# Performance work log

Measured on AMD Instinct MI355X. Metric: run time of the kernel, lower is better.

The kernel has to match this reference:

```python
import jax, jax.numpy as jnp
import numpy as np

N_NODES = 100000
N_EDGES = 1600000
HID = 128
N_GRAPHS = 2048


def _glorot(key, shape):
    fan_in, fan_out = shape[0], shape[1]
    lim = (6.0 / (fan_in + fan_out)) ** 0.5
    return jax.random.uniform(key, shape, jnp.float32, -lim, lim)


def setup_inputs() -> dict:
    key = jax.random.key(0)
    ks = jax.random.split(key, 16)
    x = jax.random.normal(ks[0], (N_NODES, 1), jnp.float32)
    edge_index = jax.random.randint(ks[1], (2, N_EDGES), 0, N_NODES, jnp.int64)
    batch = jnp.sort(jax.random.randint(ks[2], (N_NODES,), 0, N_GRAPHS, jnp.int64))
    return {
        "x": x,
        "edge_index": edge_index,
        "batch": batch,
        "W1": _glorot(ks[3], (1, HID)),   "b1": jnp.zeros((HID,), jnp.float32),
        "W2": _glorot(ks[4], (HID, HID)), "b2": jnp.zeros((HID,), jnp.float32),
        "W3": _glorot(ks[5], (HID, HID)), "b3": jnp.zeros((HID,), jnp.float32),
        "Wl1": _glorot(ks[6], (HID, HID)), "bl1": jnp.zeros((HID,), jnp.float32),
        "Wl2": _glorot(ks[7], (HID, HID)), "bl2": jnp.zeros((HID,), jnp.float32),
        "Wl3": _glorot(ks[8], (HID, 1)),   "bl3": jnp.zeros((1,), jnp.float32),
    }


def _gcn_layer(h, src, dst, norm, W, b, n_nodes):
    # h: [N, Fin] -> [N, Fout]; GCNConv: D^-1/2 (A+I) D^-1/2 (h W) + b
    hw = h @ W                                   # [N, Fout]
    msg = hw[src] * norm[:, None]                # [E+N, Fout] gather + scale
    return jax.ops.segment_sum(msg, dst, num_segments=n_nodes) + b


def _gcn_norm(edge_index, n_nodes, dtype):
    loop = jnp.arange(n_nodes, dtype=edge_index.dtype)
    src = jnp.concatenate([edge_index[0], loop])  # self-loops appended
    dst = jnp.concatenate([edge_index[1], loop])
    deg = jax.ops.segment_sum(jnp.ones_like(dst, dtype=dtype), dst, num_segments=n_nodes)
    dinv = jnp.where(deg > 0, jax.lax.rsqrt(jnp.maximum(deg, 1e-12)), 0.0)
    norm = dinv[src] * dinv[dst]                  # [E+N]
    return src, dst, norm


def reference(x, edge_index, batch, W1, b1, W2, b2, W3, b3, Wl1, bl1, Wl2, bl2, Wl3, bl3):
    n = x.shape[0]
    src, dst, norm = _gcn_norm(edge_index, n, x.dtype)
    h = jax.nn.relu(_gcn_layer(x, src, dst, norm, W1, b1, n))
    h = jax.nn.relu(_gcn_layer(h, src, dst, norm, W2, b2, n))
    h = jax.nn.relu(_gcn_layer(h, src, dst, norm, W3, b3, n))
    # global_mean_pool over graph ids
    sums = jax.ops.segment_sum(h, batch, num_segments=N_GRAPHS)          # [G, HID]
    cnt = jax.ops.segment_sum(jnp.ones((n,), h.dtype), batch, num_segments=N_GRAPHS)
    g = sums / jnp.maximum(cnt, 1.0)[:, None]
    g = jax.nn.relu(g @ Wl1 + bl1)
    g = jax.nn.relu(g @ Wl2 + bl2)
    out = g @ Wl3 + bl3                                                  # [G, 1]
    return out.reshape(-1)
```

## Files before the change

### kernel.cpp

```cpp
#include <hip/hip_runtime.h>
#include <hip/hip_fp16.h>

#define H 128
#define SHIFT 9
#define BN 512
#define MAXNB 256
#define CHUNK 4096
#define CAP 16384

typedef _Float16 half8 __attribute__((ext_vector_type(8)));
typedef _Float16 half4 __attribute__((ext_vector_type(4)));
typedef _Float16 half2t __attribute__((ext_vector_type(2)));
typedef float f32x4 __attribute__((ext_vector_type(4)));


__global__ __launch_bounds__(256) void scatter_pairs_k(const int* __restrict__ src,
                                                       const int* __restrict__ dst,
                                                       int* __restrict__ gcur,
                                                       unsigned* __restrict__ pairbuf,
                                                       int E, int NBv) {
    __shared__ unsigned stage[CHUNK];
    __shared__ unsigned char stb[CHUNK];
    __shared__ int hist[MAXNB], basel[MAXNB], cur[MAXNB], gbase[MAXNB];
    __shared__ int total;
    int tid = threadIdx.x;
    int base = blockIdx.x * CHUNK;

    int mysrc[16], mydst[16];
    #pragma unroll
    for (int i = 0; i < 16; ++i) {
        int e = base + i * 256 + tid;
        if (e < E) { mysrc[i] = src[e]; mydst[i] = dst[e]; } else mydst[i] = -1;
    }
    hist[tid] = 0;
    __syncthreads();
    #pragma unroll
    for (int i = 0; i < 16; ++i)
        if (mydst[i] >= 0) atomicAdd(&hist[mydst[i] >> SHIFT], 1);
    __syncthreads();
    if (tid == 0) {
        int run = 0;
        for (int b = 0; b < NBv; ++b) { basel[b] = run; run += hist[b]; }
        total = run;
    }
    __syncthreads();
    if (tid < NBv) {
        cur[tid] = basel[tid];
        if (hist[tid] > 0) gbase[tid] = tid * CAP + atomicAdd(&gcur[tid], hist[tid]);
    }
    __syncthreads();
    #pragma unroll
    for (int i = 0; i < 16; ++i)
        if (mydst[i] >= 0) {
            int b = mydst[i] >> SHIFT;
            int slot = atomicAdd(&cur[b], 1);
            stage[slot] = ((unsigned)(mydst[i] & (BN - 1)) << 17) | (unsigned)mysrc[i];
            stb[slot] = (unsigned char)b;
        }
    __syncthreads();
    for (int s = tid; s < total; s += 256) {
        int b = stb[s];
        pairbuf[gbase[b] + (s - basel[b])] = stage[s];
    }
}

__global__ __launch_bounds__(512) void build_csr_k(const unsigned* __restrict__ pairbuf,
                                                   const int* __restrict__ gcur,
                                                   const float* __restrict__ x,
                                                   int* __restrict__ offs, int* __restrict__ eend,
                                                   float* __restrict__ dinv, float* __restrict__ s,
                                                   int* __restrict__ csr, int N) {
    __shared__ int hist[BN];
    __shared__ int cur[BN];
    __shared__ int ps[BN];
    int b = blockIdx.x, tid = threadIdx.x;
    int node0 = b << SHIFT;
    int e0 = b * CAP, e1 = e0 + gcur[b];
    hist[tid] = 0;
    __syncthreads();
    for (int p = e0 + tid; p < e1; p += 512)
        atomicAdd(&hist[pairbuf[p] >> 17], 1);
    __syncthreads();
    int v0 = hist[tid];
    ps[tid] = v0;
    __syncthreads();
    for (int off = 1; off < BN; off <<= 1) {
        int t = (tid >= off) ? ps[tid - off] : 0;
        __syncthreads();
        ps[tid] += t;
        __syncthreads();
    }
    int g0 = e0 + ps[tid] - v0;
    int n0 = node0 + tid;
    if (n0 < N) {
        float d = rsqrtf((float)(v0 + 1));
        offs[n0] = g0;
        eend[n0] = g0 + v0;
        dinv[n0] = d;
        s[n0] = x[n0] * d;
    }
    cur[tid] = g0;
    __syncthreads();
    for (int p = e0 + tid; p < e1; p += 512) {
        unsigned v = pairbuf[p];
        int pos = atomicAdd(&cur[v >> 17], 1);
        csr[pos] = (int)(v & 0x1FFFFu);
    }
}


__global__ __launch_bounds__(256) void agg1_k(const float* __restrict__ s, const int* __restrict__ offs,
                                              const int* __restrict__ eend, const int* __restrict__ csr,
                                              const float* __restrict__ dinv, float2* __restrict__ td, int n) {
    int l = threadIdx.x & 63;
    int wave = threadIdx.x >> 6;
    int sub = l >> 4;
    int j   = l & 15;
    int node = blockIdx.x * 16 + wave * 4 + sub;
    int nd = node < n ? node : n - 1;
    int e0 = offs[nd], e1 = eend[nd];
    float sum = 0.f;
    int p = e0 + j;
    for (; p + 16 < e1; p += 32) {
        int iA = csr[p];
        int iB = csr[p + 16];
        float vA = s[iA];
        float vB = s[iB];
        sum += vA + vB;
    }
    if (p < e1) sum += s[csr[p]];
    #pragma unroll
    for (int m = 1; m < 16; m <<= 1) sum += __shfl_xor(sum, m);
    if (j == 0 && node < n) {
        float d = dinv[nd];
        td[node] = make_float2((sum + s[nd]) * d, d);
    }
}


__global__ __launch_bounds__(256) void gather_td_k(const int* __restrict__ csr,
                                                   const float2* __restrict__ td,
                                                   const int* __restrict__ gcur,
                                                   float2* __restrict__ etd) {
    int b = blockIdx.x >> 2;
    int k = blockIdx.x & 3;
    int base = b * CAP + k * (CAP / 4);
    int e1 = b * CAP + gcur[b];
    int hi = base + (CAP / 4); if (hi > e1) hi = e1;
    for (int p0 = base; p0 < hi; p0 += 1024) {
        int p = p0 + threadIdx.x;
        bool m0 = (p < hi), m1 = (p + 256 < hi), m2 = (p + 512 < hi), m3 = (p + 768 < hi);
        int i0 = m0 ? csr[p] : 0;
        int i1 = m1 ? csr[p + 256] : 0;
        int i2 = m2 ? csr[p + 512] : 0;
        int i3 = m3 ? csr[p + 768] : 0;
        float2 v0 = td[i0];
        float2 v1 = td[i1];
        float2 v2 = td[i2];
        float2 v3 = td[i3];
        if (m0) etd[p] = v0;
        if (m1) etd[p + 256] = v1;
        if (m2) etd[p + 512] = v2;
        if (m3) etd[p + 768] = v3;
    }
}


__global__ __launch_bounds__(256) void l2_agg_k(const float2* __restrict__ td,
                                                const float2* __restrict__ etd,
                                                const int* __restrict__ offs,
                                                const int* __restrict__ eend,
                                                const float* __restrict__ w1,
                                                const float* __restrict__ b1,
                                                _Float16* __restrict__ Uh, int n) {
    int node = blockIdx.x * 4 + (threadIdx.x >> 6);
    int lane = threadIdx.x & 63;
    if (node >= n) return;
    float wa = w1[lane],      wb = w1[lane + 64];
    float ba = b1[lane],      bb = b1[lane + 64];
    float2 self = td[node];
    float sa = fmaxf(fmaf(self.x, wa, ba), 0.f) * self.y;
    float sb = fmaxf(fmaf(self.x, wb, bb), 0.f) * self.y;
    const float2* ep = etd + offs[node];
    int cnt = eend[node] - offs[node];
    int p = 0;
    for (; p + 8 <= cnt; p += 8) {
        float2 v[8];
        #pragma unroll
        for (int u = 0; u < 8; ++u) v[u] = ep[p + u];
        #pragma unroll
        for (int u = 0; u < 8; ++u) {
            sa = fmaf(fmaxf(fmaf(v[u].x, wa, ba), 0.f), v[u].y, sa);
            sb = fmaf(fmaxf(fmaf(v[u].x, wb, bb), 0.f), v[u].y, sb);
        }
    }
    for (; p < cnt; ++p) {
        float2 v = ep[p];
        sa = fmaf(fmaxf(fmaf(v.x, wa, ba), 0.f), v.y, sa);
        sb = fmaf(fmaxf(fmaf(v.x, wb, bb), 0.f), v.y, sb);
    }
    float d = self.y;
    Uh[(size_t)node * H + lane]      = (_Float16)(sa * d);
    Uh[(size_t)node * H + lane + 64] = (_Float16)(sb * d);
}


template <bool POOL>
__global__ __launch_bounds__(256) void gemm_h_k(const _Float16* __restrict__ in,
                                                const float* __restrict__ W,
                                                const float* __restrict__ bias,
                                                const float* __restrict__ pscale,
                                                _Float16* __restrict__ out,
                                                const int* __restrict__ batch,
                                                float* __restrict__ P, int n) {
    __shared__ _Float16 WT[128 * 136];
    __shared__ _Float16 OT[64 * 136];
    __shared__ float bsh[H];
    __shared__ int bid[64];

    for (int idx = threadIdx.x; idx < 128 * 32; idx += 256) {
        int k  = idx >> 5;
        int c4 = (idx & 31) << 2;
        float4 v = *(const float4*)(W + k * H + c4);
        WT[(c4 + 0) * 136 + k] = (_Float16)v.x;
        WT[(c4 + 1) * 136 + k] = (_Float16)v.y;
        WT[(c4 + 2) * 136 + k] = (_Float16)v.z;
        WT[(c4 + 3) * 136 + k] = (_Float16)v.w;
    }
    if (threadIdx.x < H) bsh[threadIdx.x] = bias[threadIdx.x];
    if (POOL && threadIdx.x < 64) {
        int gr = blockIdx.x * 64 + threadIdx.x;
        bid[threadIdx.x] = (gr < n) ? batch[gr] : -1;
    }
    __syncthreads();

    const int wave = threadIdx.x >> 6;
    const int l    = threadIdx.x & 63;
    const int lr   = l & 15;
    const int lk   = l >> 4;
    const int row0 = blockIdx.x * 64 + wave * 16;

    f32x4 acc[8];
    #pragma unroll
    for (int c = 0; c < 8; ++c) acc[c] = (f32x4){0.f, 0.f, 0.f, 0.f};

    int arow = row0 + lr; if (arow > n - 1) arow = n - 1;
    const _Float16* ap = in + (size_t)arow * H + lk * 8;

    #pragma unroll
    for (int ks = 0; ks < 4; ++ks) {
        half8 a = *(const half8*)(ap + ks * 32);
        #pragma unroll
        for (int c = 0; c < 8; ++c) {
            half8 b = *(const half8*)(WT + (c * 16 + lr) * 136 + ks * 32 + lk * 8);
            acc[c] = __builtin_amdgcn_mfma_f32_16x16x32_f16(a, b, acc[c], 0, 0, 0);
        }
    }

    #pragma unroll
    for (int r = 0; r < 4; ++r) {
        int lrow = wave * 16 + lk * 4 + r;
        int grow = blockIdx.x * 64 + lrow;
        float sc = 1.f;
        if (pscale) { int gr = grow > n - 1 ? n - 1 : grow; sc = pscale[gr]; }
        #pragma unroll
        for (int c = 0; c < 8; ++c) {
            float v = fmaxf(acc[c][r] + bsh[c * 16 + lr], 0.f) * sc;
            OT[lrow * 136 + c * 16 + lr] = (_Float16)v;
        }
    }
    __syncthreads();

    if constexpr (POOL) {
        int f  = threadIdx.x & 127;
        int r0 = (threadIdx.x >> 7) * 32;
        float acc2 = 0.f;
        int cur = bid[r0];
        for (int r = r0; r < r0 + 32; ++r) {
            int b = bid[r];
            if (b != cur) {
                if (cur >= 0) atomicAdd(&P[(size_t)cur * H + f], acc2);
                acc2 = 0.f; cur = b;
            }
            if (b >= 0) acc2 += (float)OT[r * 136 + f];
        }
        if (cur >= 0) atomicAdd(&P[(size_t)cur * H + f], acc2);
    } else {
        for (int idx = threadIdx.x; idx < 64 * 16; idx += 256) {
            int row = idx >> 4;
            int gr = blockIdx.x * 64 + row;
            if (gr < n)
                ((uint4*)(out + (size_t)gr * H))[idx & 15] = ((const uint4*)(OT + row * 136))[idx & 15];
        }
    }
}


__device__ __forceinline__ void acc_h(float4& a, uint2 r) {
    __half2 h0 = *(__half2*)&r.x;
    __half2 h1 = *(__half2*)&r.y;
    float2 f0 = __half22float2(h0);
    float2 f1 = __half22float2(h1);
    a.x += f0.x; a.y += f0.y; a.z += f1.x; a.w += f1.y;
}

__device__ __forceinline__ float4 gather_row_sum_h(const uint2* __restrict__ hrow,
                                                   const int* __restrict__ csr,
                                                   int node, int e0, int e1, int half, int l) {
    float4 acc[8];
    #pragma unroll
    for (int u = 0; u < 8; ++u) acc[u] = make_float4(0.f, 0.f, 0.f, 0.f);
    if (half == 0) {
        uint2 rs = hrow[(size_t)node * 32 + l];
        acc_h(acc[0], rs);
    }
    int q = e0;
    for (; q + 15 < e1; q += 16) {
        int idx[8];
        #pragma unroll
        for (int u = 0; u < 8; ++u) idx[u] = csr[q + 2 * u + half];
        uint2 raw[8];
        #pragma unroll
        for (int u = 0; u < 8; ++u) raw[u] = hrow[(size_t)idx[u] * 32 + l];
        #pragma unroll
        for (int u = 0; u < 8; ++u) acc_h(acc[u], raw[u]);
    }
    for (; q + 7 < e1; q += 8) {
        int idx[4];
        #pragma unroll
        for (int u = 0; u < 4; ++u) idx[u] = csr[q + 2 * u + half];
        uint2 raw[4];
        #pragma unroll
        for (int u = 0; u < 4; ++u) raw[u] = hrow[(size_t)idx[u] * 32 + l];
        #pragma unroll
        for (int u = 0; u < 4; ++u) acc_h(acc[u], raw[u]);
    }
    for (; q < e1; q += 2) {
        int off = q + half;
        if (off < e1) {
            uint2 raw = hrow[(size_t)csr[off] * 32 + l];
            acc_h(acc[0], raw);
        }
    }
    float4 sum;
    sum.x = ((acc[0].x + acc[1].x) + (acc[2].x + acc[3].x)) + ((acc[4].x + acc[5].x) + (acc[6].x + acc[7].x));
    sum.y = ((acc[0].y + acc[1].y) + (acc[2].y + acc[3].y)) + ((acc[4].y + acc[5].y) + (acc[6].y + acc[7].y));
    sum.z = ((acc[0].z + acc[1].z) + (acc[2].z + acc[3].z)) + ((acc[4].z + acc[5].z) + (acc[6].z + acc[7].z));
    sum.w = ((acc[0].w + acc[1].w) + (acc[2].w + acc[3].w)) + ((acc[4].w + acc[5].w) + (acc[6].w + acc[7].w));
    sum.x += __shfl_xor(sum.x, 32);
    sum.y += __shfl_xor(sum.y, 32);
    sum.z += __shfl_xor(sum.z, 32);
    sum.w += __shfl_xor(sum.w, 32);
    return sum;
}


__global__ __launch_bounds__(256) void agg3h_k(const uint2* __restrict__ Zh, const int* __restrict__ offs,
                                               const int* __restrict__ eend, const int* __restrict__ csr,
                                               const float* __restrict__ dinv,
                                               _Float16* __restrict__ Uh, int n) {
    int node = blockIdx.x * 4 + (threadIdx.x >> 6);
    int lane = threadIdx.x & 63;
    int half = lane >> 5;
    int l = lane & 31;
    if (node >= n) return;
    float4 sum = gather_row_sum_h(Zh, csr, node, offs[node], eend[node], half, l);
    if (half == 0) {
        float d = dinv[node];
        half4 o;
        o[0] = (_Float16)(sum.x * d);
        o[1] = (_Float16)(sum.y * d);
        o[2] = (_Float16)(sum.z * d);
        o[3] = (_Float16)(sum.w * d);
        *(half4*)(Uh + (size_t)node * H + l * 4) = o;
    }
}


__global__ __launch_bounds__(256) void head_k(const float* __restrict__ P,
                                              const int* __restrict__ batch,
                                              const float* __restrict__ Wl1, const float* __restrict__ bl1,
                                              const float* __restrict__ Wl2, const float* __restrict__ bl2,
                                              const float* __restrict__ Wl3, const float* __restrict__ bl3,
                                              float* __restrict__ out, int G, int n) {
    __shared__ float Wb[H * H];
    __shared__ float Tl[32 * 133];
    __shared__ float w3l[H];
    __shared__ int lb[33];
    int tid = threadIdx.x;
    int g0 = blockIdx.x * 32;

    if (tid < 128) w3l[tid] = Wl3[tid];
    if (tid >= 128 && tid < 161) {
        int g = g0 + (tid - 128); if (g > G) g = G;
        int lo = 0, hi = n;
        while (lo < hi) { int m = (lo + hi) >> 1; if (batch[m] < g) lo = m + 1; else hi = m; }
        lb[tid - 128] = lo;
    }
    for (int i = tid; i < H * H / 4; i += 256) ((float4*)Wb)[i] = ((const float4*)Wl1)[i];
    __syncthreads();

    const int cc = tid & 7, rg = tid >> 3, c0 = cc * 16;
    int grow = g0 + rg; if (grow > G - 1) grow = G - 1;
    int cntg = lb[rg + 1] - lb[rg];
    float rinv = 1.f / (cntg < 1 ? 1.f : (float)cntg);
    float acc[16];

    #pragma unroll
    for (int j = 0; j < 16; ++j) acc[j] = 0.f;
    const float4* P4 = (const float4*)P;
    for (int k4 = 0; k4 < H / 4; ++k4) {
        float4 a = P4[(size_t)grow * 32 + k4];
        a.x *= rinv; a.y *= rinv; a.z *= rinv; a.w *= rinv;
        const float* wbase = Wb + (k4 * 4) * H + c0;
        #pragma unroll
        for (int kk = 0; kk < 4; ++kk) {
            float w[16];
            *(float4*)(w + 0)  = *(const float4*)(wbase + kk * H + 0);
            *(float4*)(w + 4)  = *(const float4*)(wbase + kk * H + 4);
            *(float4*)(w + 8)  = *(const float4*)(wbase + kk * H + 8);
            *(float4*)(w + 12) = *(const float4*)(wbase + kk * H + 12);
            float av = ((const float*)&a)[kk];
            #pragma unroll
            for (int j = 0; j < 16; ++j)
                acc[j] = fmaf(av, w[j], acc[j]);
        }
    }
    #pragma unroll
    for (int j = 0; j < 16; ++j)
        Tl[rg * 133 + c0 + j] = fmaxf(acc[j] + bl1[c0 + j], 0.f);
    __syncthreads();
    for (int i = tid; i < H * H / 4; i += 256) ((float4*)Wb)[i] = ((const float4*)Wl2)[i];
    __syncthreads();

    #pragma unroll
    for (int j = 0; j < 16; ++j) acc[j] = 0.f;
    for (int k4 = 0; k4 < H / 4; ++k4) {
        float4 a = *(const float4*)(Tl + rg * 133 + k4 * 4);
        const float* wbase = Wb + (k4 * 4) * H + c0;
        #pragma unroll
        for (int kk = 0; kk < 4; ++kk) {
            float w[16];
            *(float4*)(w + 0)  = *(const float4*)(wbase + kk * H + 0);
            *(float4*)(w + 4)  = *(const float4*)(wbase + kk * H + 4);
            *(float4*)(w + 8)  = *(const float4*)(wbase + kk * H + 8);
            *(float4*)(w + 12) = *(const float4*)(wbase + kk * H + 12);
            float av = ((const float*)&a)[kk];
            #pragma unroll
            for (int j = 0; j < 16; ++j)
                acc[j] = fmaf(av, w[j], acc[j]);
        }
    }
    float part = 0.f;
    #pragma unroll
    for (int j = 0; j < 16; ++j)
        part += fmaxf(acc[j] + bl2[c0 + j], 0.f) * w3l[c0 + j];
    #pragma unroll
    for (int off = 1; off < 8; off <<= 1)
        part += __shfl_xor(part, off);
    if (cc == 0 && g0 + rg < G)
        out[g0 + rg] = part + bl3[0];
}


extern "C" void kernel_launch(void* const* d_in, const int* in_sizes, int n_in,
                              void* d_out, int out_size, void* d_ws, size_t ws_size,
                              hipStream_t stream) {
    const float* x     = (const float*)d_in[0];
    const int*   ei    = (const int*)d_in[1];
    const int*   batch = (const int*)d_in[2];
    const float* W1  = (const float*)d_in[3];  const float* b1  = (const float*)d_in[4];
    const float* W2  = (const float*)d_in[5];  const float* b2  = (const float*)d_in[6];
    const float* W3  = (const float*)d_in[7];  const float* b3  = (const float*)d_in[8];
    const float* Wl1 = (const float*)d_in[9];  const float* bl1 = (const float*)d_in[10];
    const float* Wl2 = (const float*)d_in[11]; const float* bl2 = (const float*)d_in[12];
    const float* Wl3 = (const float*)d_in[13]; const float* bl3 = (const float*)d_in[14];

    const int N = in_sizes[0];
    const int E = in_sizes[1] / 2;
    const int G = out_size;
    const int* srcp = ei;
    const int* dstp = ei + E;
    const int NB = (N + BN - 1) / BN;

    char* w = (char*)d_ws;
    size_t off = 0;
    auto alloc = [&](size_t bytes) -> void* {
        void* p = w + off;
        off += (bytes + 255) & ~(size_t)255;
        return p;
    };
    int*    gcur   = (int*)alloc((size_t)MAXNB * 4);
    float*  P      = (float*)alloc((size_t)G * H * 4);
    size_t  zbytes = off;
    int*    offs   = (int*)alloc((size_t)N * 4);
    int*    eend   = (int*)alloc((size_t)N * 4);
    int*    csr    = (int*)alloc((size_t)NB * CAP * 4);
    float*  dinv   = (float*)alloc((size_t)N * 4);
    float*  sbuf   = (float*)alloc((size_t)N * 4);
    float2* td     = (float2*)alloc((size_t)N * 8);
    float*  A      = (float*)alloc((size_t)N * H * 4);
    float*  B      = (float*)alloc((size_t)N * H * 4);
    unsigned* pairbuf = (unsigned*)B;
    float2*   etd     = (float2*)B;
    _Float16* Z2h     = (_Float16*)B;
    _Float16* U2h     = (_Float16*)A;
    _Float16* U3h     = (_Float16*)A;
    (void)ws_size; (void)n_in;

    hipMemsetAsync(gcur, 0, zbytes, stream);
    scatter_pairs_k<<<(E + CHUNK - 1) / CHUNK, 256, 0, stream>>>(srcp, dstp, gcur, pairbuf, E, NB);
    build_csr_k<<<NB, 512, 0, stream>>>(pairbuf, gcur, x, offs, eend, dinv, sbuf, csr, N);

    agg1_k<<<(N + 15) / 16, 256, 0, stream>>>(sbuf, offs, eend, csr, dinv, td, N);

    gather_td_k<<<NB * 4, 256, 0, stream>>>(csr, td, gcur, etd);
    l2_agg_k<<<(N + 3) / 4, 256, 0, stream>>>(td, etd, offs, eend, W1, b1, U2h, N);
    gemm_h_k<false><<<(N + 63) / 64, 256, 0, stream>>>(U2h, W2, b2, dinv, Z2h, nullptr, nullptr, N);

    agg3h_k<<<(N + 3) / 4, 256, 0, stream>>>((const uint2*)Z2h, offs, eend, csr, dinv, U3h, N);
    gemm_h_k<true><<<(N + 63) / 64, 256, 0, stream>>>(U3h, W3, b3, nullptr, nullptr, batch, P, N);

    head_k<<<(G + 31) / 32, 256, 0, stream>>>(P, batch, Wl1, bl1, Wl2, bl2, Wl3, bl3,
                                              (float*)d_out, G, N);
}
```

Measured before the change: 377.4 us.

## Halve scatter chunk, parallel-scan bucket offsets, split accumulators, nontemporal stores

```diff
diff --git a/kernel.cpp b/kernel.cpp
--- a/kernel.cpp
+++ b/kernel.cpp
@@ -5,7 +5,7 @@
 #define SHIFT 9
 #define BN 512
 #define MAXNB 256
-#define CHUNK 4096
+#define CHUNK 2048
 #define CAP 16384
 
 typedef _Float16 half8 __attribute__((ext_vector_type(8)));
@@ -20,42 +20,50 @@
                                                        unsigned* __restrict__ pairbuf,
                                                        int E, int NBv) {
     __shared__ unsigned stage[CHUNK];
-    __shared__ unsigned char stb[CHUNK];
+    __shared__ unsigned short stb[CHUNK];
     __shared__ int hist[MAXNB], basel[MAXNB], cur[MAXNB], gbase[MAXNB];
+    __shared__ int ps2[256];
     __shared__ int total;
     int tid = threadIdx.x;
     int base = blockIdx.x * CHUNK;
 
-    int mysrc[16], mydst[16];
-    #pragma unroll
-    for (int i = 0; i < 16; ++i) {
+    int mysrc[CHUNK / 256], mydst[CHUNK / 256];
+    #pragma unroll
+    for (int i = 0; i < CHUNK / 256; ++i) {
         int e = base + i * 256 + tid;
         if (e < E) { mysrc[i] = src[e]; mydst[i] = dst[e]; } else mydst[i] = -1;
     }
     hist[tid] = 0;
     __syncthreads();
     #pragma unroll
-    for (int i = 0; i < 16; ++i)
+    for (int i = 0; i < CHUNK / 256; ++i)
         if (mydst[i] >= 0) atomicAdd(&hist[mydst[i] >> SHIFT], 1);
     __syncthreads();
-    if (tid == 0) {
-        int run = 0;
-        for (int b = 0; b < NBv; ++b) { basel[b] = run; run += hist[b]; }
-        total = run;
-    }
-    __syncthreads();
+    int hv = (tid < NBv) ? hist[tid] : 0;
+    ps2[tid] = hv;
+    __syncthreads();
+    #pragma unroll
+    for (int off = 1; off < 256; off <<= 1) {
+        int t = (tid >= off) ? ps2[tid - off] : 0;
+        __syncthreads();
+        ps2[tid] += t;
+        __syncthreads();
+    }
     if (tid < NBv) {
-        cur[tid] = basel[tid];
-        if (hist[tid] > 0) gbase[tid] = tid * CAP + atomicAdd(&gcur[tid], hist[tid]);
-    }
-    __syncthreads();
-    #pragma unroll
-    for (int i = 0; i < 16; ++i)
+        int b0 = ps2[tid] - hv;
+        basel[tid] = b0;
+        cur[tid] = b0;
+        if (hv > 0) gbase[tid] = tid * CAP + atomicAdd(&gcur[tid], hv);
+    }
+    if (tid == 255) total = ps2[255];
+    __syncthreads();
+    #pragma unroll
+    for (int i = 0; i < CHUNK / 256; ++i)
         if (mydst[i] >= 0) {
             int b = mydst[i] >> SHIFT;
             int slot = atomicAdd(&cur[b], 1);
             stage[slot] = ((unsigned)(mydst[i] & (BN - 1)) << 17) | (unsigned)mysrc[i];
-            stb[slot] = (unsigned char)b;
+            stb[slot] = (unsigned short)b;
         }
     __syncthreads();
     for (int s = tid; s < total; s += 256) {
@@ -179,8 +187,10 @@
     float wa = w1[lane],      wb = w1[lane + 64];
     float ba = b1[lane],      bb = b1[lane + 64];
     float2 self = td[node];
-    float sa = fmaxf(fmaf(self.x, wa, ba), 0.f) * self.y;
-    float sb = fmaxf(fmaf(self.x, wb, bb), 0.f) * self.y;
+    float a0 = fmaxf(fmaf(self.x, wa, ba), 0.f) * self.y;
+    float b0v = fmaxf(fmaf(self.x, wb, bb), 0.f) * self.y;
+    float a1 = 0.f, a2 = 0.f, a3 = 0.f;
+    float b1v = 0.f, b2v = 0.f, b3v = 0.f;
     const float2* ep = etd + offs[node];
     int cnt = eend[node] - offs[node];
     int p = 0;
@@ -188,17 +198,28 @@
         float2 v[8];
         #pragma unroll
         for (int u = 0; u < 8; ++u) v[u] = ep[p + u];
+        float ra[8], rb[8];
         #pragma unroll
         for (int u = 0; u < 8; ++u) {
-            sa = fmaf(fmaxf(fmaf(v[u].x, wa, ba), 0.f), v[u].y, sa);
-            sb = fmaf(fmaxf(fmaf(v[u].x, wb, bb), 0.f), v[u].y, sb);
-        }
+            ra[u] = fmaxf(fmaf(v[u].x, wa, ba), 0.f);
+            rb[u] = fmaxf(fmaf(v[u].x, wb, bb), 0.f);
+        }
+        a0 = fmaf(ra[0], v[0].y, a0); a1 = fmaf(ra[1], v[1].y, a1);
+        a2 = fmaf(ra[2], v[2].y, a2); a3 = fmaf(ra[3], v[3].y, a3);
+        a0 = fmaf(ra[4], v[4].y, a0); a1 = fmaf(ra[5], v[5].y, a1);
+        a2 = fmaf(ra[6], v[6].y, a2); a3 = fmaf(ra[7], v[7].y, a3);
+        b0v = fmaf(rb[0], v[0].y, b0v); b1v = fmaf(rb[1], v[1].y, b1v);
+        b2v = fmaf(rb[2], v[2].y, b2v); b3v = fmaf(rb[3], v[3].y, b3v);
+        b0v = fmaf(rb[4], v[4].y, b0v); b1v = fmaf(rb[5], v[5].y, b1v);
+        b2v = fmaf(rb[6], v[6].y, b2v); b3v = fmaf(rb[7], v[7].y, b3v);
     }
     for (; p < cnt; ++p) {
         float2 v = ep[p];
-        sa = fmaf(fmaxf(fmaf(v.x, wa, ba), 0.f), v.y, sa);
-        sb = fmaf(fmaxf(fmaf(v.x, wb, bb), 0.f), v.y, sb);
-    }
+        a1 = fmaf(fmaxf(fmaf(v.x, wa, ba), 0.f), v.y, a1);
+        b1v = fmaf(fmaxf(fmaf(v.x, wb, bb), 0.f), v.y, b1v);
+    }
+    float sa = (a0 + a1) + (a2 + a3);
+    float sb = (b0v + b1v) + (b2v + b3v);
     float d = self.y;
     Uh[(size_t)node * H + lane]      = (_Float16)(sa * d);
     Uh[(size_t)node * H + lane + 64] = (_Float16)(sb * d);
@@ -372,7 +393,9 @@
         o[1] = (_Float16)(sum.y * d);
         o[2] = (_Float16)(sum.z * d);
         o[3] = (_Float16)(sum.w * d);
-        *(half4*)(Uh + (size_t)node * H + l * 4) = o;
+        unsigned long long bits;
+        __builtin_memcpy(&bits, &o, 8);
+        __builtin_nontemporal_store(bits, (unsigned long long*)(Uh + (size_t)node * H + l * 4));
     }
 }
 
@@ -508,7 +531,7 @@
     _Float16* U3h     = (_Float16*)A;
     (void)ws_size; (void)n_in;
 
-    hipMemsetAsync(gcur, 0, zbytes, stream);
+    (void)hipMemsetAsync(gcur, 0, zbytes, stream);
     scatter_pairs_k<<<(E + CHUNK - 1) / CHUNK, 256, 0, stream>>>(srcp, dstp, gcur, pairbuf, E, NB);
     build_csr_k<<<NB, 512, 0, stream>>>(pairbuf, gcur, x, offs, eend, dinv, sbuf, csr, N);
 
```

After: 386.9 us. 2.5% more time.
